# Kernel tuning notes

Hardware: AMD Instinct MI355X
Metric: run time of the kernel (lower is better)

The kernel has to match this reference:

```python
import jax, jax.numpy as jnp
import numpy as np

B, L, N, DOUT = 8, 8192, 256, 256  # batch, seq_len, state_dim, output_dim


def setup_inputs() -> dict:
    key = jax.random.key(0)
    k_u, k_h, k_w = jax.random.split(key, 3)
    u = jax.random.normal(k_u, (B, L, 1), dtype=jnp.float32)
    # impulse response buffer (stands in for A_bar^i @ B_bar rows); decay-scaled for realism
    h = jax.random.normal(k_h, (L, N), dtype=jnp.float32) * 0.02
    W = jax.random.normal(k_w, (DOUT, N), dtype=jnp.float32) * (1.0 / np.sqrt(N))
    return {"u": u, "h": h, "W": W}


def reference(u, h, W):
    L_ = h.shape[0]
    n_fft = 2 * L_
    # FFT-based long convolution: U:[B, n_fft//2+1, 1], H:[n_fft//2+1, N]
    U = jnp.fft.rfft(u, n=n_fft, axis=1)
    H = jnp.fft.rfft(h, n=n_fft, axis=0)
    M = U * H[None, :, :]                      # broadcast channel 1 -> N
    m = jnp.fft.irfft(M, n=n_fft, axis=1)[:, :L_, :]  # [B, L, N]
    return jnp.einsum('bln,on->blo', m, W)     # Linear(state_dim -> output_dim), no bias
```

## Files before the change

### kernel.cpp

```cpp
#include <hip/hip_runtime.h>
#include <hip/hip_bf16.h>
#include <stdint.h>
#include <stddef.h>

typedef __attribute__((ext_vector_type(4))) float f32x4;
typedef __attribute__((ext_vector_type(8))) short s16x8;

#define B_    8
#define L_    8192
#define N_    256
#define DOUT_ 256
#define M_    8192
#define GSTRIDE 8200
#define RC    0.70710678118654752f
#define C8    0.92387953251128675613f
#define S8    0.38268343236508977173f

__device__ __forceinline__ unsigned short f2bf(float f) {
  unsigned int x = __float_as_uint(f);
  x += 0x7fff + ((x >> 16) & 1);
  return (unsigned short)(x >> 16);
}

__device__ __forceinline__ float2 cmul(float2 a, float2 b) {
  return make_float2(a.x * b.x - a.y * b.y, a.x * b.y + a.y * b.x);
}
__device__ __forceinline__ float2 cadd(float2 a, float2 b) { return make_float2(a.x + b.x, a.y + b.y); }
__device__ __forceinline__ float2 csub(float2 a, float2 b) { return make_float2(a.x - b.x, a.y - b.y); }

__device__ __forceinline__ int phi(int i) {
  return i ^ ((((i >> 4) ^ (i >> 7) ^ (i >> 10)) & 7) << 1);
}
__device__ __forceinline__ int rev13(int i) { return (int)(__brev((unsigned)i) >> 19); }

template<bool INV> __device__ __forceinline__ float2 twmul(float2 x, float2 w) {
  return INV ? make_float2(x.x * w.x + x.y * w.y, x.y * w.x - x.x * w.y)
             : make_float2(x.x * w.x - x.y * w.y, x.x * w.y + x.y * w.x);
}
template<bool INV> __device__ __forceinline__ float2 mul_mi(float2 x) {
  return INV ? make_float2(-x.y, x.x) : make_float2(x.y, -x.x);
}
template<bool INV> __device__ __forceinline__ float2 mul_w8(float2 x) {
  return INV ? make_float2(RC * (x.x - x.y), RC * (x.x + x.y))
             : make_float2(RC * (x.x + x.y), RC * (x.y - x.x));
}
template<bool INV> __device__ __forceinline__ float2 mul_w83(float2 x) {
  return INV ? make_float2(-RC * (x.x + x.y), RC * (x.x - x.y))
             : make_float2(RC * (x.y - x.x), -RC * (x.x + x.y));
}

template<bool INV>
__device__ __forceinline__ void r16(float2* a, float2 wA, float2 wB, float2 wC, float2 wD) {
  float2 b[16];
#pragma unroll
  for (int k = 0; k < 8; ++k) {
    b[k] = cadd(a[k], a[k + 8]);
    float2 t = twmul<INV>(csub(a[k], a[k + 8]), wA);
    if (k == 1) t = twmul<INV>(t, make_float2(C8, -S8));
    else if (k == 2) t = mul_w8<INV>(t);
    else if (k == 3) t = twmul<INV>(t, make_float2(S8, -C8));
    else if (k == 4) t = mul_mi<INV>(t);
    else if (k == 5) t = twmul<INV>(t, make_float2(-S8, -C8));
    else if (k == 6) t = mul_w83<INV>(t);
    else if (k == 7) t = twmul<INV>(t, make_float2(-C8, -S8));
    b[k + 8] = t;
  }
  float2 c[16];
#pragma unroll
  for (int blk = 0; blk < 16; blk += 8)
#pragma unroll
    for (int k = 0; k < 4; ++k) {
      c[blk + k] = cadd(b[blk + k], b[blk + k + 4]);
      float2 t = twmul<INV>(csub(b[blk + k], b[blk + k + 4]), wB);
      if (k == 1) t = mul_w8<INV>(t);
      else if (k == 2) t = mul_mi<INV>(t);
      else if (k == 3) t = mul_w83<INV>(t);
      c[blk + k + 4] = t;
    }
  float2 d[16];
#pragma unroll
  for (int blk = 0; blk < 16; blk += 4)
#pragma unroll
    for (int k = 0; k < 2; ++k) {
      d[blk + k] = cadd(c[blk + k], c[blk + k + 2]);
      float2 t = twmul<INV>(csub(c[blk + k], c[blk + k + 2]), wC);
      if (k == 1) t = mul_mi<INV>(t);
      d[blk + k + 2] = t;
    }
#pragma unroll
  for (int blk = 0; blk < 16; blk += 2) {
    a[blk]     = cadd(d[blk], d[blk + 1]);
    a[blk + 1] = twmul<INV>(csub(d[blk], d[blk + 1]), wD);
  }
}

__device__ __forceinline__ void preload_tw(const float2* __restrict__ tw, int tid, float2* twp) {
  const int p0 = tid, p1 = tid & 31, p2 = tid & 1;
  twp[0] = tw[p0 << 1];  twp[1] = tw[p0 << 2];  twp[2]  = tw[p0 << 3];  twp[3]  = tw[p0 << 4];
  twp[4] = tw[p1 << 5];  twp[5] = tw[p1 << 6];  twp[6]  = tw[p1 << 7];  twp[7]  = tw[p1 << 8];
  twp[8] = tw[p2 << 9];  twp[9] = tw[p2 << 10]; twp[10] = tw[p2 << 11]; twp[11] = tw[p2 << 12];
}

#define FFT_PASS(INV, SH, BASE, W0, W1, W2, W3) do { \
    const int base_ = (BASE); \
    float2 a_[16]; \
    _Pragma("unroll") \
    for (int k = 0; k < 16; ++k) a_[k] = zc[phi(base_ + (k << (SH)))]; \
    r16<INV>(a_, W0, W1, W2, W3); \
    _Pragma("unroll") \
    for (int k = 0; k < 16; ++k) zc[phi(base_ + (k << (SH)))] = a_[k]; \
  } while (0)

template<bool INV>
__device__ __forceinline__ void fft12(float2* zc, int tid, const float2* twp) {
  FFT_PASS(INV, 9, tid, twp[0], twp[1], twp[2], twp[3]);
  __syncthreads();
  FFT_PASS(INV, 5, ((tid >> 5) << 9) + (tid & 31), twp[4], twp[5], twp[6], twp[7]);
  __syncthreads();
  FFT_PASS(INV, 1, ((tid >> 1) << 5) + (tid & 1), twp[8], twp[9], twp[10], twp[11]);
  __syncthreads();
}

__global__ void k_tw(float2* __restrict__ tw) {
  int k = blockIdx.x * 256 + threadIdx.x;
  float a = (float)k * 3.8349519697141029e-4f;
  tw[k] = make_float2(__cosf(a), -__sinf(a));
}

__global__ void k_gt(const float* __restrict__ W, const float* __restrict__ h,
                     unsigned short* __restrict__ gT) {
  int gid  = blockIdx.x * 256 + threadIdx.x;
  int lane = gid & 63;
  int wid  = gid >> 6;
  int o_t  = wid >> 7;
  int i_t  = wid & 127;
  int o0 = o_t * 16, i0 = i_t * 64;
  int ln = lane & 15, hi = lane >> 4;
  f32x4 acc[4] = {};
#pragma unroll
  for (int k0 = 0; k0 < N_; k0 += 32) {
    const float* wp = W + (o0 + ln) * N_ + k0 + 8 * hi;
    float4 w0 = *(const float4*)wp;
    float4 w1 = *(const float4*)(wp + 4);
    s16x8 a;
    a[0] = (short)f2bf(w0.x); a[1] = (short)f2bf(w0.y);
    a[2] = (short)f2bf(w0.z); a[3] = (short)f2bf(w0.w);
    a[4] = (short)f2bf(w1.x); a[5] = (short)f2bf(w1.y);
    a[6] = (short)f2bf(w1.z); a[7] = (short)f2bf(w1.w);
#pragma unroll
    for (int ns = 0; ns < 4; ++ns) {
      const float* hp = h + (size_t)(i0 + 16 * ns + ln) * N_ + k0 + 8 * hi;
      float4 h0 = *(const float4*)hp;
      float4 h1 = *(const float4*)(hp + 4);
      s16x8 bb;
      bb[0] = (short)f2bf(h0.x); bb[1] = (short)f2bf(h0.y);
      bb[2] = (short)f2bf(h0.z); bb[3] = (short)f2bf(h0.w);
      bb[4] = (short)f2bf(h1.x); bb[5] = (short)f2bf(h1.y);
      bb[6] = (short)f2bf(h1.z); bb[7] = (short)f2bf(h1.w);
      acc[ns] = __builtin_amdgcn_mfma_f32_16x16x32_bf16(a, bb, acc[ns], 0, 0, 0);
    }
  }
#pragma unroll
  for (int ns = 0; ns < 4; ++ns)
#pragma unroll
    for (int q = 0; q < 4; ++q)
      gT[(size_t)(o0 + 4 * hi + q) * L_ + i0 + 16 * ns + ln] = f2bf(acc[ns][q]);
}

__global__ __launch_bounds__(512, 4) void k_ffwd(const float* __restrict__ u,
                                                 const unsigned short* __restrict__ gT,
                                                 const float2* __restrict__ tw,
                                                 float2* __restrict__ U,
                                                 float2* __restrict__ G) {
  __shared__ __align__(16) float2 zc[M_];
  const int wg = blockIdx.x;
  const int tid = threadIdx.x;
  float2 twp[12];
  preload_tw(tw, tid, twp);

  if (wg < 8) {
    const float2* src = (const float2*)(u + wg * L_);
#pragma unroll 4
    for (int kp = 0; kp < 16; ++kp) {
      int t = tid + 512 * kp;
      zc[phi(t)] = (t < 4096) ? src[t] : make_float2(0.f, 0.f);
    }
  } else {
    const unsigned int* src = (const unsigned int*)(gT + (size_t)(wg - 8) * L_);
#pragma unroll 4
    for (int kp = 0; kp < 16; ++kp) {
      int t = tid + 512 * kp;
      float2 v = make_float2(0.f, 0.f);
      if (t < 4096) {
        unsigned int pr = src[t];
        v.x = __uint_as_float(pr << 16);
        v.y = __uint_as_float(pr & 0xffff0000u);
      }
      zc[phi(t)] = v;
    }
  }
  __syncthreads();

  fft12<false>(zc, tid, twp);

  float2* dst = (wg < 8) ? (U + (size_t)wg * GSTRIDE) : (G + (size_t)(wg - 8) * GSTRIDE);
#pragma unroll 4
  for (int kp = 0; kp < 16; ++kp) {
    int k = tid + 512 * kp;
    int m1 = rev13(k);
    int m2 = rev13((M_ - k) & (M_ - 1));
    float4 v1 = *(const float4*)(zc + phi(m1 & ~1));
    float4 v2 = *(const float4*)(zc + phi(m2 & ~1));
    float2 zk  = (m1 & 1) ? make_float2(v1.x - v1.z, v1.y - v1.w)
                          : make_float2(v1.x + v1.z, v1.y + v1.w);
    float2 zmk = (m2 & 1) ? make_float2(v2.x - v2.z, v2.y - v2.w)
                          : make_float2(v2.x + v2.z, v2.y + v2.w);
    float2 E = make_float2(0.5f * (zk.x + zmk.x), 0.5f * (zk.y - zmk.y));
    float2 O = make_float2(0.5f * (zk.y + zmk.y), 0.5f * (zmk.x - zk.x));
    float2 w = tw[k];
    float2 X = cmul(w, O);
    dst[k] = make_float2(E.x + X.x, E.y + X.y);
  }
  if (tid == 0) {
    float4 v = *(const float4*)zc;
    float2 z0 = make_float2(v.x + v.z, v.y + v.w);
    dst[M_] = make_float2(z0.x - z0.y, 0.f);
  }
}

__global__ __launch_bounds__(512, 4) void k_conv(const float2* __restrict__ U,
                                                 const float2* __restrict__ G,
                                                 const float2* __restrict__ tw,
                                                 float* __restrict__ out) {
  __shared__ __align__(16) float2 zc[M_];
  const int bid = blockIdx.x;
  const int widx = (bid & 7) * 256 + (bid >> 3);
  const int b = widx >> 8;
  const int o = widx & 255;
  const int tid = threadIdx.x;
  const float2* Ub = U + (size_t)b * GSTRIDE;
  const float2* Go = G + (size_t)o * GSTRIDE;
  float2 twp[12];
  preload_tw(tw, tid, twp);

#pragma unroll 2
  for (int kp = 0; kp < 8; ++kp) {
    int k = tid + 512 * kp;
    float2 Yk = cmul(Ub[k], Go[k]);
    if (k == 0) {
      float2 Ym = cmul(Ub[M_], Go[M_]);
      float2 E = make_float2(0.5f * (Yk.x + Ym.x), 0.5f * (Yk.y - Ym.y));
      float2 D = make_float2(0.5f * (Yk.x - Ym.x), 0.5f * (Yk.y + Ym.y));
      zc[0] = make_float2(E.x - D.y, E.y + D.x);
      float2 Y4 = cmul(Ub[4096], Go[4096]);
      zc[phi(4096)] = make_float2(Y4.x, -Y4.y);
    } else {
      float2 Ymk = cmul(Ub[M_ - k], Go[M_ - k]);
      float2 E = make_float2(0.5f * (Yk.x + Ymk.x), 0.5f * (Yk.y - Ymk.y));
      float2 D = make_float2(0.5f * (Yk.x - Ymk.x), 0.5f * (Yk.y + Ymk.y));
      float2 w = tw[k];
      float2 O = make_float2(D.x * w.x + D.y * w.y, -D.x * w.y + D.y * w.x);
      zc[phi(k)]      = make_float2(E.x - O.y,  E.y + O.x);
      zc[phi(M_ - k)] = make_float2(E.x + O.y, -E.y + O.x);
    }
  }
  __syncthreads();

  fft12<true>(zc, tid, twp);

  const float s1 = 1.0f / 8192.0f;
  float* ob = out + (size_t)b * (L_ * DOUT_) + o;
#pragma unroll 2
  for (int kp = 0; kp < 8; ++kp) {
    int t = tid + 512 * kp;
    int m = rev13(t);
    float4 v = *(const float4*)(zc + phi(m));
    ob[(size_t)(2 * t) * DOUT_]     = (v.x + v.z) * s1;
    ob[(size_t)(2 * t + 1) * DOUT_] = (v.y + v.w) * s1;
  }
}

extern "C" void kernel_launch(void* const* d_in, const int* in_sizes, int n_in,
                              void* d_out, int out_size, void* d_ws, size_t ws_size,
                              hipStream_t stream) {
  const float* u = (const float*)d_in[0];
  const float* h = (const float*)d_in[1];
  const float* W = (const float*)d_in[2];
  float* out = (float*)d_out;

  char* ws = (char*)d_ws;
  unsigned short* gT = (unsigned short*)ws;
  float2* tw = (float2*)(ws + (size_t)4 * 1024 * 1024);
  float2* U  = (float2*)(ws + (size_t)4 * 1024 * 1024 + 65536);
  float2* G  = (float2*)(ws + (size_t)4 * 1024 * 1024 + 65536 + 524800);

  k_tw<<<32, 256, 0, stream>>>(tw);
  k_gt<<<512, 256, 0, stream>>>(W, h, gT);
  k_ffwd<<<264, 512, 0, stream>>>(u, gT, tw, U, G);
  k_conv<<<2048, 512, 0, stream>>>(U, G, tw, out);
}
```

Before: 187.5 us.

## Process two output channels per conv block with paired FFTs and vectorized stores

Each k_conv block now handles two output channels for the same batch. It reuses the U spectrum loads and shares twiddles and index computation across two interleaved inverse FFTs in LDS, and writes adjacent outputs as float2 stores. The 1/8192 normalization moves into the forward G spectrum. Doubling LDS to 128KB per block lowers occupancy to 2 blocks per CU, and the grid is halved.

```diff
diff --git a/kernel.cpp b/kernel.cpp
--- a/kernel.cpp
+++ b/kernel.cpp
@@ -120,6 +120,24 @@
   FFT_PASS(INV, 1, ((tid >> 1) << 5) + (tid & 1), twp[8], twp[9], twp[10], twp[11]);
   __syncthreads();
 }
+
+#define FFT_PASS2(INV, SH, BASE, W0, W1, W2, W3) do { \
+    const int base_ = (BASE); \
+    int ix_[16]; \
+    _Pragma("unroll") \
+    for (int k = 0; k < 16; ++k) ix_[k] = phi(base_ + (k << (SH))); \
+    float2 aA_[16], aB_[16]; \
+    _Pragma("unroll") \
+    for (int k = 0; k < 16; ++k) aA_[k] = zA[ix_[k]]; \
+    _Pragma("unroll") \
+    for (int k = 0; k < 16; ++k) aB_[k] = zB[ix_[k]]; \
+    r16<INV>(aA_, W0, W1, W2, W3); \
+    _Pragma("unroll") \
+    for (int k = 0; k < 16; ++k) zA[ix_[k]] = aA_[k]; \
+    r16<INV>(aB_, W0, W1, W2, W3); \
+    _Pragma("unroll") \
+    for (int k = 0; k < 16; ++k) zB[ix_[k]] = aB_[k]; \
+  } while (0)
 
 __global__ void k_tw(float2* __restrict__ tw) {
   int k = blockIdx.x * 256 + threadIdx.x;
@@ -203,6 +221,7 @@
 
   fft12<false>(zc, tid, twp);
 
+  const float sc = (wg < 8) ? 1.0f : (1.0f / 8192.0f);
   float2* dst = (wg < 8) ? (U + (size_t)wg * GSTRIDE) : (G + (size_t)(wg - 8) * GSTRIDE);
 #pragma unroll 4
   for (int kp = 0; kp < 16; ++kp) {
@@ -219,64 +238,88 @@
     float2 O = make_float2(0.5f * (zk.y + zmk.y), 0.5f * (zmk.x - zk.x));
     float2 w = tw[k];
     float2 X = cmul(w, O);
-    dst[k] = make_float2(E.x + X.x, E.y + X.y);
+    dst[k] = make_float2((E.x + X.x) * sc, (E.y + X.y) * sc);
   }
   if (tid == 0) {
     float4 v = *(const float4*)zc;
     float2 z0 = make_float2(v.x + v.z, v.y + v.w);
-    dst[M_] = make_float2(z0.x - z0.y, 0.f);
-  }
-}
-
-__global__ __launch_bounds__(512, 4) void k_conv(const float2* __restrict__ U,
+    dst[M_] = make_float2((z0.x - z0.y) * sc, 0.f);
+  }
+}
+
+__global__ __launch_bounds__(512, 2) void k_conv(const float2* __restrict__ U,
                                                  const float2* __restrict__ G,
                                                  const float2* __restrict__ tw,
                                                  float* __restrict__ out) {
-  __shared__ __align__(16) float2 zc[M_];
+  __shared__ __align__(16) float2 zA[M_];
+  __shared__ __align__(16) float2 zB[M_];
   const int bid = blockIdx.x;
-  const int widx = (bid & 7) * 256 + (bid >> 3);
-  const int b = widx >> 8;
-  const int o = widx & 255;
+  const int b = bid & 7;
+  const int o0 = (bid >> 3) * 2;
   const int tid = threadIdx.x;
   const float2* Ub = U + (size_t)b * GSTRIDE;
-  const float2* Go = G + (size_t)o * GSTRIDE;
+  const float2* GA = G + (size_t)o0 * GSTRIDE;
+  const float2* GB = GA + GSTRIDE;
   float2 twp[12];
   preload_tw(tw, tid, twp);
 
 #pragma unroll 2
   for (int kp = 0; kp < 8; ++kp) {
     int k = tid + 512 * kp;
-    float2 Yk = cmul(Ub[k], Go[k]);
+    float2 Uk = Ub[k];
+    float2 YA = cmul(Uk, GA[k]);
+    float2 YB = cmul(Uk, GB[k]);
     if (k == 0) {
-      float2 Ym = cmul(Ub[M_], Go[M_]);
-      float2 E = make_float2(0.5f * (Yk.x + Ym.x), 0.5f * (Yk.y - Ym.y));
-      float2 D = make_float2(0.5f * (Yk.x - Ym.x), 0.5f * (Yk.y + Ym.y));
-      zc[0] = make_float2(E.x - D.y, E.y + D.x);
-      float2 Y4 = cmul(Ub[4096], Go[4096]);
-      zc[phi(4096)] = make_float2(Y4.x, -Y4.y);
+      float2 Um = Ub[M_];
+      float2 YAm = cmul(Um, GA[M_]);
+      float2 YBm = cmul(Um, GB[M_]);
+      float2 EA = make_float2(0.5f * (YA.x + YAm.x), 0.5f * (YA.y - YAm.y));
+      float2 DA = make_float2(0.5f * (YA.x - YAm.x), 0.5f * (YA.y + YAm.y));
+      float2 EB = make_float2(0.5f * (YB.x + YBm.x), 0.5f * (YB.y - YBm.y));
+      float2 DB = make_float2(0.5f * (YB.x - YBm.x), 0.5f * (YB.y + YBm.y));
+      zA[0] = make_float2(EA.x - DA.y, EA.y + DA.x);
+      zB[0] = make_float2(EB.x - DB.y, EB.y + DB.x);
+      float2 U4 = Ub[4096];
+      float2 YA4 = cmul(U4, GA[4096]);
+      float2 YB4 = cmul(U4, GB[4096]);
+      zA[phi(4096)] = make_float2(YA4.x, -YA4.y);
+      zB[phi(4096)] = make_float2(YB4.x, -YB4.y);
     } else {
-      float2 Ymk = cmul(Ub[M_ - k], Go[M_ - k]);
-      float2 E = make_float2(0.5f * (Yk.x + Ymk.x), 0.5f * (Yk.y - Ymk.y));
-      float2 D = make_float2(0.5f * (Yk.x - Ymk.x), 0.5f * (Yk.y + Ymk.y));
+      float2 Umk = Ub[M_ - k];
+      float2 YAm = cmul(Umk, GA[M_ - k]);
+      float2 YBm = cmul(Umk, GB[M_ - k]);
       float2 w = tw[k];
-      float2 O = make_float2(D.x * w.x + D.y * w.y, -D.x * w.y + D.y * w.x);
-      zc[phi(k)]      = make_float2(E.x - O.y,  E.y + O.x);
-      zc[phi(M_ - k)] = make_float2(E.x + O.y, -E.y + O.x);
-    }
-  }
-  __syncthreads();
-
-  fft12<true>(zc, tid, twp);
-
-  const float s1 = 1.0f / 8192.0f;
-  float* ob = out + (size_t)b * (L_ * DOUT_) + o;
+      float2 EA = make_float2(0.5f * (YA.x + YAm.x), 0.5f * (YA.y - YAm.y));
+      float2 DA = make_float2(0.5f * (YA.x - YAm.x), 0.5f * (YA.y + YAm.y));
+      float2 OA = make_float2(DA.x * w.x + DA.y * w.y, -DA.x * w.y + DA.y * w.x);
+      zA[phi(k)]      = make_float2(EA.x - OA.y,  EA.y + OA.x);
+      zA[phi(M_ - k)] = make_float2(EA.x + OA.y, -EA.y + OA.x);
+      float2 EB = make_float2(0.5f * (YB.x + YBm.x), 0.5f * (YB.y - YBm.y));
+      float2 DB = make_float2(0.5f * (YB.x - YBm.x), 0.5f * (YB.y + YBm.y));
+      float2 OB = make_float2(DB.x * w.x + DB.y * w.y, -DB.x * w.y + DB.y * w.x);
+      zB[phi(k)]      = make_float2(EB.x - OB.y,  EB.y + OB.x);
+      zB[phi(M_ - k)] = make_float2(EB.x + OB.y, -EB.y + OB.x);
+    }
+  }
+  __syncthreads();
+
+  FFT_PASS2(true, 9, tid, twp[0], twp[1], twp[2], twp[3]);
+  __syncthreads();
+  FFT_PASS2(true, 5, ((tid >> 5) << 9) + (tid & 31), twp[4], twp[5], twp[6], twp[7]);
+  __syncthreads();
+  FFT_PASS2(true, 1, ((tid >> 1) << 5) + (tid & 1), twp[8], twp[9], twp[10], twp[11]);
+  __syncthreads();
+
+  float* ob = out + (size_t)b * (L_ * DOUT_) + o0;
 #pragma unroll 2
   for (int kp = 0; kp < 8; ++kp) {
     int t = tid + 512 * kp;
     int m = rev13(t);
-    float4 v = *(const float4*)(zc + phi(m));
-    ob[(size_t)(2 * t) * DOUT_]     = (v.x + v.z) * s1;
-    ob[(size_t)(2 * t + 1) * DOUT_] = (v.y + v.w) * s1;
+    int sm = phi(m);
+    float4 vA = *(const float4*)(zA + sm);
+    float4 vB = *(const float4*)(zB + sm);
+    *(float2*)(ob + (size_t)(2 * t) * DOUT_)     = make_float2(vA.x + vA.z, vB.x + vB.z);
+    *(float2*)(ob + (size_t)(2 * t + 1) * DOUT_) = make_float2(vA.y + vA.w, vB.y + vB.w);
   }
 }
 
@@ -297,5 +340,5 @@
   k_tw<<<32, 256, 0, stream>>>(tw);
   k_gt<<<512, 256, 0, stream>>>(W, h, gT);
   k_ffwd<<<264, 512, 0, stream>>>(u, gT, tw, U, G);
-  k_conv<<<2048, 512, 0, stream>>>(U, G, tw, out);
-}
+  k_conv<<<1024, 512, 0, stream>>>(U, G, tw, out);
+}
```

After: 197.5 us. +5.4%, slower.
